# Optimization experiments

Measured on AMD Instinct MI355X. Metric: run time of the kernel, lower is better.

Reference implementation:

```python
import jax, jax.numpy as jnp
import numpy as np

N_NODES = 50000
N_EDGES = 1600000
F_IN = 128
HID = 128
N_CLS = 16


def setup_inputs() -> dict:
    key = jax.random.key(0)
    ks = jax.random.split(key, 8)
    x = jax.random.normal(ks[0], (N_NODES, F_IN), dtype=jnp.float32)
    edge_index = jax.random.randint(ks[1], (2, N_EDGES), 0, N_NODES, dtype=jnp.int64)
    W1 = jax.random.normal(ks[2], (F_IN, HID), dtype=jnp.float32) * (1.0 / np.sqrt(F_IN))
    b1 = jnp.zeros((HID,), dtype=jnp.float32)
    W2 = jax.random.normal(ks[3], (HID, HID), dtype=jnp.float32) * (1.0 / np.sqrt(HID))
    b2 = jnp.zeros((HID,), dtype=jnp.float32)
    W3 = jax.random.normal(ks[4], (HID, N_CLS), dtype=jnp.float32) * (1.0 / np.sqrt(HID))
    b3 = jnp.zeros((N_CLS,), dtype=jnp.float32)
    return {"x": x, "edge_index": edge_index, "W1": W1, "b1": b1,
            "W2": W2, "b2": b2, "W3": W3, "b3": b3}


def _gcn_norm(edge_index, n_nodes, dtype):
    # PyG gcn_norm with add_self_loops=True, improved=False
    loops = jnp.arange(n_nodes, dtype=edge_index.dtype)
    row = jnp.concatenate([edge_index[0], loops])  # source j
    col = jnp.concatenate([edge_index[1], loops])  # target i
    deg = jax.ops.segment_sum(jnp.ones(row.shape[0], dtype=dtype), col,
                              num_segments=n_nodes)
    dinv = jnp.where(deg > 0, jax.lax.rsqrt(deg), 0.0)
    norm = dinv[row] * dinv[col]  # [E + N]
    return row, col, norm


def _gcn_conv(h, W, b, row, col, norm, n_nodes):
    h = h @ W                              # [N, out] linear first (PyG order)
    msg = h[row] * norm[:, None]           # gather + per-edge scale
    agg = jax.ops.segment_sum(msg, col, num_segments=n_nodes)  # scatter-add
    return agg + b


def reference(x, edge_index, W1, b1, W2, b2, W3, b3):
    n = x.shape[0]
    row, col, norm = _gcn_norm(edge_index, n, x.dtype)
    h = jax.nn.relu(_gcn_conv(x, W1, b1, row, col, norm, n))
    h = jax.nn.relu(_gcn_conv(h, W2, b2, row, col, norm, n))
    h = jax.nn.relu(_gcn_conv(h, W3, b3, row, col, norm, n))
    return h
```

## Files before the change

kernel.cpp:

```cpp
#include <hip/hip_runtime.h>
#include <hip/hip_fp16.h>


static inline int cdiv(int a, int b) { return (a + b - 1) / b; }

__global__ __launch_bounds__(256) void k_zero_int(int* p, int n) {
    int i = blockIdx.x * 256 + threadIdx.x;
    if (i < n) p[i] = 0;
}

__global__ __launch_bounds__(256) void k_count(const int* __restrict__ col, int* cnt, int e) {
    int i = blockIdx.x * 256 + threadIdx.x;
    if (i < e) atomicAdd(&cnt[col[i]], 1);
}

__global__ __launch_bounds__(256) void k_scanA(const int* __restrict__ cnt, int* bsum,
                                               float* __restrict__ dinv, int n) {
    __shared__ int s[256];
    int t = threadIdx.x;
    int i = blockIdx.x * 256 + t;
    int v = (i < n) ? cnt[i] : 0;
    if (i < n) dinv[i] = rsqrtf((float)(v + 1));
    s[t] = v;
    __syncthreads();
    for (int off = 128; off > 0; off >>= 1) {
        if (t < off) s[t] += s[t + off];
        __syncthreads();
    }
    if (t == 0) bsum[blockIdx.x] = s[0];
}

__global__ __launch_bounds__(256) void k_scanB(int* bsum, int nb) {
    __shared__ int s[256];
    int t = threadIdx.x;
    int v = (t < nb) ? bsum[t] : 0;
    s[t] = v;
    for (int off = 1; off < 256; off <<= 1) {
        __syncthreads();
        int x = (t >= off) ? s[t - off] : 0;
        __syncthreads();
        s[t] += x;
    }
    __syncthreads();
    if (t < nb) bsum[t] = s[t] - v;
}

__global__ __launch_bounds__(256) void k_scanC(const int* __restrict__ cnt, const int* __restrict__ bsum,
                                               int* offs, int* cur, int n) {
    __shared__ int s[256];
    int t = threadIdx.x;
    int i = blockIdx.x * 256 + t;
    int v = (i < n) ? cnt[i] : 0;
    s[t] = v;
    for (int off = 1; off < 256; off <<= 1) {
        __syncthreads();
        int x = (t >= off) ? s[t - off] : 0;
        __syncthreads();
        s[t] += x;
    }
    __syncthreads();
    int ov = bsum[blockIdx.x] + s[t] - v;
    if (i <= n) offs[i] = ov;
    if (i < n) cur[i] = ov;
}

__global__ __launch_bounds__(256) void k_fill(const int* __restrict__ row, const int* __restrict__ col,
                                              const float* __restrict__ dinv, int* cur,
                                              unsigned int* __restrict__ csr, int e) {
    int i = blockIdx.x * 256 + threadIdx.x;
    if (i >= e) return;
    int c = col[i], r = row[i];
    float w = dinv[r] * dinv[c];
    int pos = atomicAdd(&cur[c], 1);
    unsigned short hw = __half_as_ushort(__float2half_rn(w));
    csr[pos] = ((unsigned int)r << 16) | (unsigned int)hw;
}

__global__ __launch_bounds__(256) void k_gemm128(const float* __restrict__ X, const float* __restrict__ W,
                                                 __half* __restrict__ Ah, int n) {
    __shared__ float sW[128 * 128];
    __shared__ float sX[16][128];
    int tid = threadIdx.x;
    for (int i = tid; i < 4096; i += 256)
        ((float4*)sW)[i] = ((const float4*)W)[i];

    int row0 = blockIdx.x * 128;
    int tx = tid & 15, ty = tid >> 4;
    float acc[8][8];
    #pragma unroll
    for (int i = 0; i < 8; ++i)
        #pragma unroll
        for (int j = 0; j < 8; ++j) acc[i][j] = 0.f;

    for (int k0 = 0; k0 < 128; k0 += 16) {
        __syncthreads();
        #pragma unroll
        for (int i = tid; i < 512; i += 256) {
            int r = i >> 2, kq = i & 3;
            int gr = row0 + r;
            float4 v = (gr < n) ? ((const float4*)X)[(size_t)gr * 32 + (k0 >> 2) + kq]
                                : make_float4(0.f, 0.f, 0.f, 0.f);
            sX[kq * 4 + 0][r] = v.x;
            sX[kq * 4 + 1][r] = v.y;
            sX[kq * 4 + 2][r] = v.z;
            sX[kq * 4 + 3][r] = v.w;
        }
        __syncthreads();
        #pragma unroll
        for (int kk = 0; kk < 16; ++kk) {
            float a[8], b[8];
            *(float4*)&a[0] = *(const float4*)&sX[kk][ty * 8];
            *(float4*)&a[4] = *(const float4*)&sX[kk][ty * 8 + 4];
            *(float4*)&b[0] = *(const float4*)&sW[(k0 + kk) * 128 + tx * 8];
            *(float4*)&b[4] = *(const float4*)&sW[(k0 + kk) * 128 + tx * 8 + 4];
            #pragma unroll
            for (int i = 0; i < 8; ++i)
                #pragma unroll
                for (int j = 0; j < 8; ++j)
                    acc[i][j] = fmaf(a[i], b[j], acc[i][j]);
        }
    }
    #pragma unroll
    for (int i = 0; i < 8; ++i) {
        int gr = row0 + ty * 8 + i;
        if (gr < n) {
            union { uint4 u; __half2 h[4]; } pk;
            pk.h[0] = __floats2half2_rn(acc[i][0], acc[i][1]);
            pk.h[1] = __floats2half2_rn(acc[i][2], acc[i][3]);
            pk.h[2] = __floats2half2_rn(acc[i][4], acc[i][5]);
            pk.h[3] = __floats2half2_rn(acc[i][6], acc[i][7]);
            ((uint4*)Ah)[(size_t)gr * 16 + tx] = pk.u;
        }
    }
}

__global__ __launch_bounds__(256) void k_gemm16(const float* __restrict__ X, const float* __restrict__ W,
                                                __half* __restrict__ Ch, int n) {
    __shared__ float sX[16 * 132];
    __shared__ float sW[128 * 16];
    int tid = threadIdx.x;
    for (int i = tid; i < 512; i += 256)
        ((float4*)sW)[i] = ((const float4*)W)[i];
    int row0 = blockIdx.x * 16;
    for (int i = tid; i < 512; i += 256) {
        int r = i >> 5, c = i & 31;
        int gr = row0 + r;
        float4 v = (gr < n) ? ((const float4*)X)[(size_t)gr * 32 + c]
                            : make_float4(0.f, 0.f, 0.f, 0.f);
        *(float4*)&sX[r * 132 + c * 4] = v;
    }
    __syncthreads();

    int rl = tid >> 4, cj = tid & 15;
    float acc = 0.f;
    #pragma unroll 8
    for (int k = 0; k < 128; ++k)
        acc = fmaf(sX[rl * 132 + k], sW[k * 16 + cj], acc);
    int gr = row0 + rl;
    if (gr < n) Ch[(size_t)gr * 16 + cj] = __float2half_rn(acc);
}

__global__ __launch_bounds__(256) void k_agg128(const __half* __restrict__ Hh, const unsigned int* __restrict__ csr,
                                                const int* __restrict__ offs, const float* __restrict__ dinv,
                                                const float* __restrict__ b, float* __restrict__ out, int n) {
    int node = (blockIdx.x * 256 + threadIdx.x) >> 6;
    if (node >= n) return;
    int lane = threadIdx.x & 63;
    int sub  = lane & 31;
    int half = lane >> 5;
    const uint2* H2 = (const uint2*)Hh;
    int ed = offs[node], end = offs[node + 1];
    float4 acc = make_float4(0.f, 0.f, 0.f, 0.f);

    #define EDGE_FMA(P)                                                          \
        {                                                                        \
            uint2 q = H2[(size_t)((P) >> 16) * 32 + sub];                        \
            float w = __half2float(__ushort_as_half((unsigned short)((P) & 0xffffu))); \
            float2 f01 = __half22float2(*(const __half2*)&q.x);                  \
            float2 f23 = __half22float2(*(const __half2*)&q.y);                  \
            acc.x = fmaf(w, f01.x, acc.x); acc.y = fmaf(w, f01.y, acc.y);        \
            acc.z = fmaf(w, f23.x, acc.z); acc.w = fmaf(w, f23.y, acc.w);        \
        }

    for (; ed + 7 < end; ed += 8) {
        unsigned int p0 = csr[ed     + half];
        unsigned int p1 = csr[ed + 2 + half];
        unsigned int p2 = csr[ed + 4 + half];
        unsigned int p3 = csr[ed + 6 + half];
        EDGE_FMA(p0); EDGE_FMA(p1); EDGE_FMA(p2); EDGE_FMA(p3);
    }
    #pragma unroll
    for (int s = 0; s < 4; ++s) {
        int idx = ed + 2 * s + half;
        if (idx < end) {
            unsigned int p = csr[idx];
            EDGE_FMA(p);
        }
    }
    #undef EDGE_FMA

    acc.x += __shfl_xor(acc.x, 32);
    acc.y += __shfl_xor(acc.y, 32);
    acc.z += __shfl_xor(acc.z, 32);
    acc.w += __shfl_xor(acc.w, 32);

    float di = dinv[node], sl = di * di;
    uint2 qh = H2[(size_t)node * 32 + sub];
    float2 h01 = __half22float2(*(const __half2*)&qh.x);
    float2 h23 = __half22float2(*(const __half2*)&qh.y);
    float4 bv = ((const float4*)b)[sub];
    float4 o;
    o.x = fmaxf(fmaf(sl, h01.x, acc.x) + bv.x, 0.f);
    o.y = fmaxf(fmaf(sl, h01.y, acc.y) + bv.y, 0.f);
    o.z = fmaxf(fmaf(sl, h23.x, acc.z) + bv.z, 0.f);
    o.w = fmaxf(fmaf(sl, h23.y, acc.w) + bv.w, 0.f);
    if (half == 0)
        ((float4*)out)[(size_t)node * 32 + sub] = o;
}

__global__ __launch_bounds__(256) void k_agg16(const __half* __restrict__ Ch, const unsigned int* __restrict__ csr,
                                               const int* __restrict__ offs, const float* __restrict__ dinv,
                                               const float* __restrict__ b, float* __restrict__ out, int n) {
    int t = blockIdx.x * 256 + threadIdx.x;
    int node = t >> 3;
    if (node >= n) return;
    int lane = t & 7;
    int sub  = lane & 3;
    int half = lane >> 2;
    const uint2* C2 = (const uint2*)Ch;
    int ed = offs[node], end = offs[node + 1];
    float4 acc = make_float4(0.f, 0.f, 0.f, 0.f);

    #define EDGE_FMA16(P)                                                        \
        {                                                                        \
            uint2 q = C2[(size_t)((P) >> 16) * 4 + sub];                         \
            float w = __half2float(__ushort_as_half((unsigned short)((P) & 0xffffu))); \
            float2 f01 = __half22float2(*(const __half2*)&q.x);                  \
            float2 f23 = __half22float2(*(const __half2*)&q.y);                  \
            acc.x = fmaf(w, f01.x, acc.x); acc.y = fmaf(w, f01.y, acc.y);        \
            acc.z = fmaf(w, f23.x, acc.z); acc.w = fmaf(w, f23.y, acc.w);        \
        }

    for (; ed + 3 < end; ed += 4) {
        unsigned int p0 = csr[ed     + half];
        unsigned int p1 = csr[ed + 2 + half];
        EDGE_FMA16(p0); EDGE_FMA16(p1);
    }
    #pragma unroll
    for (int s = 0; s < 2; ++s) {
        int idx = ed + 2 * s + half;
        if (idx < end) {
            unsigned int p = csr[idx];
            EDGE_FMA16(p);
        }
    }
    #undef EDGE_FMA16

    acc.x += __shfl_xor(acc.x, 4);
    acc.y += __shfl_xor(acc.y, 4);
    acc.z += __shfl_xor(acc.z, 4);
    acc.w += __shfl_xor(acc.w, 4);

    float di = dinv[node], sl = di * di;
    uint2 qh = C2[(size_t)node * 4 + sub];
    float2 h01 = __half22float2(*(const __half2*)&qh.x);
    float2 h23 = __half22float2(*(const __half2*)&qh.y);
    float4 bv = ((const float4*)b)[sub];
    float4 o;
    o.x = fmaxf(fmaf(sl, h01.x, acc.x) + bv.x, 0.f);
    o.y = fmaxf(fmaf(sl, h01.y, acc.y) + bv.y, 0.f);
    o.z = fmaxf(fmaf(sl, h23.x, acc.z) + bv.z, 0.f);
    o.w = fmaxf(fmaf(sl, h23.y, acc.w) + bv.w, 0.f);
    if (half == 0)
        ((float4*)out)[(size_t)node * 4 + sub] = o;
}

extern "C" void kernel_launch(void* const* d_in, const int* in_sizes, int n_in,
                              void* d_out, int out_size, void* d_ws, size_t ws_size,
                              hipStream_t stream) {
    const float* x  = (const float*)d_in[0];
    const int*   ei = (const int*)d_in[1];
    const float* W1 = (const float*)d_in[2];
    const float* b1 = (const float*)d_in[3];
    const float* W2 = (const float*)d_in[4];
    const float* b2 = (const float*)d_in[5];
    const float* W3 = (const float*)d_in[6];
    const float* b3 = (const float*)d_in[7];

    const int n = in_sizes[0] / 128;
    const int e = in_sizes[1] / 2;
    const int* row = ei;
    const int* col = ei + e;

    unsigned int* csr = (unsigned int*)d_ws;
    __half* Ah  = (__half*)(csr + e);
    float*  B   = (float*)(Ah + (size_t)n * 128);
    __half* Ch  = (__half*)(B + (size_t)n * 128);
    float* dinv = (float*)(Ch + (size_t)n * 16);
    int*   offs = (int*)(dinv + n);
    int*   cnt  = offs + (n + 1);
    int*   cur  = cnt + n;
    int*   bsum = cur + n;
    float* out  = (float*)d_out;

    const int nb = cdiv(n + 1, 256);

    k_zero_int<<<cdiv(n, 256), 256, 0, stream>>>(cnt, n);
    k_count   <<<cdiv(e, 256), 256, 0, stream>>>(col, cnt, e);
    k_scanA   <<<nb, 256, 0, stream>>>(cnt, bsum, dinv, n);
    k_scanB   <<<1, 256, 0, stream>>>(bsum, nb);
    k_scanC   <<<nb, 256, 0, stream>>>(cnt, bsum, offs, cur, n);
    k_fill    <<<cdiv(e, 256), 256, 0, stream>>>(row, col, dinv, cur, csr, e);

    k_gemm128<<<cdiv(n, 128), 256, 0, stream>>>(x, W1, Ah, n);
    k_agg128 <<<cdiv(n * 64, 256), 256, 0, stream>>>(Ah, csr, offs, dinv, b1, B, n);
    k_gemm128<<<cdiv(n, 128), 256, 0, stream>>>(B, W2, Ah, n);
    k_agg128 <<<cdiv(n * 64, 256), 256, 0, stream>>>(Ah, csr, offs, dinv, b2, B, n);
    k_gemm16 <<<cdiv(n, 16), 256, 0, stream>>>(B, W3, Ch, n);
    k_agg16  <<<cdiv(n * 8, 256), 256, 0, stream>>>(Ch, csr, offs, dinv, b3, out, n);
}
```

Baseline: 381.3 us.

## Two-pass bucketed CSR fill to localize scatter atomics into node ranges

Replaces the single-pass CSR fill, which scatters atomics and writes across the whole array, with two passes. The first pass partitions edges into 8 destination-node ranges using shared-memory staging buffers and bulk flushes. The second pass fills CSR one range at a time, so per-node atomic counters and writes stay within a smaller, more cache-resident region. This costs an extra kernel, an extra temporary edge array pass, and block-wide syncs in the bucketing loop.

```diff
diff --git a/kernel.cpp b/kernel.cpp
--- a/kernel.cpp
+++ b/kernel.cpp
@@ -46,7 +46,7 @@
 }
 
 __global__ __launch_bounds__(256) void k_scanC(const int* __restrict__ cnt, const int* __restrict__ bsum,
-                                               int* offs, int* cur, int n) {
+                                               int* offs, int* cur, int* gcur, int rs, int n) {
     __shared__ int s[256];
     int t = threadIdx.x;
     int i = blockIdx.x * 256 + t;
@@ -61,19 +61,81 @@
     __syncthreads();
     int ov = bsum[blockIdx.x] + s[t] - v;
     if (i <= n) offs[i] = ov;
-    if (i < n) cur[i] = ov;
-}
-
-__global__ __launch_bounds__(256) void k_fill(const int* __restrict__ row, const int* __restrict__ col,
-                                              const float* __restrict__ dinv, int* cur,
-                                              unsigned int* __restrict__ csr, int e) {
-    int i = blockIdx.x * 256 + threadIdx.x;
-    if (i >= e) return;
-    int c = col[i], r = row[i];
-    float w = dinv[r] * dinv[c];
-    int pos = atomicAdd(&cur[c], 1);
-    unsigned short hw = __half_as_ushort(__float2half_rn(w));
-    csr[pos] = ((unsigned int)r << 16) | (unsigned int)hw;
+    if (i < n) {
+        cur[i] = ov;
+        if ((i % rs) == 0) gcur[i / rs] = ov;
+    }
+}
+
+__global__ __launch_bounds__(256) void k_bucket(const int* __restrict__ row, const int* __restrict__ col,
+                                                int* gcur, unsigned int* __restrict__ tmp,
+                                                int e, int rs, int nblk) {
+    __shared__ unsigned int buf[8][512];
+    __shared__ int bcnt[8];
+    __shared__ int bbase[8];
+    int tid = threadIdx.x;
+    if (tid < 8) bcnt[tid] = 0;
+    __syncthreads();
+    int stride = nblk * 256;
+    for (int base = blockIdx.x * 256; base < e; base += stride) {
+        int i = base + tid;
+        if (i < e) {
+            int c = col[i], r = row[i];
+            int g = c / rs;
+            int slot = atomicAdd(&bcnt[g], 1);
+            buf[g][slot] = ((unsigned int)(c - g * rs) << 16) | (unsigned int)r;
+        }
+        __syncthreads();
+        #pragma unroll
+        for (int g = 0; g < 8; ++g) {
+            int c8 = bcnt[g];
+            if (c8 >= 256) {
+                if (tid == 0) bbase[g] = atomicAdd(&gcur[g], c8);
+                __syncthreads();
+                int gb = bbase[g];
+                for (int k = tid; k < c8; k += 256)
+                    tmp[gb + k] = buf[g][k];
+                __syncthreads();
+                if (tid == 0) bcnt[g] = 0;
+                __syncthreads();
+            }
+        }
+        __syncthreads();
+    }
+    #pragma unroll
+    for (int g = 0; g < 8; ++g) {
+        int c8 = bcnt[g];
+        if (c8 > 0) {
+            if (tid == 0) bbase[g] = atomicAdd(&gcur[g], c8);
+            __syncthreads();
+            int gb = bbase[g];
+            for (int k = tid; k < c8; k += 256)
+                tmp[gb + k] = buf[g][k];
+            __syncthreads();
+        }
+    }
+}
+
+__global__ __launch_bounds__(256) void k_fillB(const unsigned int* __restrict__ tmp,
+                                               const float* __restrict__ dinv,
+                                               const int* __restrict__ offs, int* cur,
+                                               unsigned int* __restrict__ csr,
+                                               int n, int rs, int nblk) {
+    int g = blockIdx.x & 7;
+    int b = blockIdx.x >> 3;
+    int base = g * rs;
+    int en = min(base + rs, n);
+    int s0 = offs[base], s1 = offs[en];
+    int stride = nblk * 256;
+    for (int i = s0 + b * 256 + threadIdx.x; i < s1; i += stride) {
+        unsigned int u = tmp[i];
+        int r = (int)(u & 0xffffu);
+        int c = base + (int)(u >> 16);
+        float w = dinv[r] * dinv[c];
+        int pos = atomicAdd(&cur[c], 1);
+        csr[pos] = ((unsigned int)r << 16) |
+                   (unsigned int)__half_as_ushort(__float2half_rn(w));
+    }
 }
 
 __global__ __launch_bounds__(256) void k_gemm128(const float* __restrict__ X, const float* __restrict__ W,
@@ -291,9 +353,11 @@
     const int e = in_sizes[1] / 2;
     const int* row = ei;
     const int* col = ei + e;
+    const int rs = (n + 7) >> 3;
 
     unsigned int* csr = (unsigned int*)d_ws;
-    __half* Ah  = (__half*)(csr + e);
+    unsigned int* tmp = csr + e;
+    __half* Ah  = (__half*)(tmp + e);
     float*  B   = (float*)(Ah + (size_t)n * 128);
     __half* Ch  = (__half*)(B + (size_t)n * 128);
     float* dinv = (float*)(Ch + (size_t)n * 16);
@@ -301,16 +365,20 @@
     int*   cnt  = offs + (n + 1);
     int*   cur  = cnt + n;
     int*   bsum = cur + n;
+    int*   gcur = bsum + 256;
     float* out  = (float*)d_out;
 
     const int nb = cdiv(n + 1, 256);
+    const int bucketBlocks = 1024;
+    const int fillBBlocks  = 128;
 
     k_zero_int<<<cdiv(n, 256), 256, 0, stream>>>(cnt, n);
     k_count   <<<cdiv(e, 256), 256, 0, stream>>>(col, cnt, e);
     k_scanA   <<<nb, 256, 0, stream>>>(cnt, bsum, dinv, n);
     k_scanB   <<<1, 256, 0, stream>>>(bsum, nb);
-    k_scanC   <<<nb, 256, 0, stream>>>(cnt, bsum, offs, cur, n);
-    k_fill    <<<cdiv(e, 256), 256, 0, stream>>>(row, col, dinv, cur, csr, e);
+    k_scanC   <<<nb, 256, 0, stream>>>(cnt, bsum, offs, cur, gcur, rs, n);
+    k_bucket  <<<bucketBlocks, 256, 0, stream>>>(row, col, gcur, tmp, e, rs, bucketBlocks);
+    k_fillB   <<<8 * fillBBlocks, 256, 0, stream>>>(tmp, dinv, offs, cur, csr, n, rs, fillBBlocks);
 
     k_gemm128<<<cdiv(n, 128), 256, 0, stream>>>(x, W1, Ah, n);
     k_agg128 <<<cdiv(n * 64, 256), 256, 0, stream>>>(Ah, csr, offs, dinv, b1, B, n);
```

After: 462.1 us. +21.2%, slower.
